# Kernel optimization log

Hardware: AMD Instinct MI355X
Metric: run time of the kernel (lower is better)

The kernel has to match this reference:

```python
import jax, jax.numpy as jnp
import numpy as np

SR = 44100
DUR = 2.0
DS = 64
IN_GAIN = 10.0 ** (5.2 / 20.0)


def design_lr4_ir(freq, sr, n_taps=512):
    wc = np.tan(np.pi * freq / sr)
    wc2 = wc * wc
    root2 = np.sqrt(2.0)
    denom = 1 + root2 * wc + wc2
    b_lp = np.array([wc2 / denom, 2 * wc2 / denom, wc2 / denom])
    a_lp = np.array([1.0, 2 * (wc2 - 1) / denom, (1 - root2 * wc + wc2) / denom])
    b_hp = np.array([1 / denom, -2 / denom, 1 / denom])
    a_hp = np.array([1.0, 2 * (wc2 - 1) / denom, (1 - root2 * wc + wc2) / denom])
    b_lp4 = np.convolve(b_lp, b_lp); a_lp4 = np.convolve(a_lp, a_lp)
    b_hp4 = np.convolve(b_hp, b_hp); a_hp4 = np.convolve(a_hp, a_hp)
    def lfilter(b, a, x):
        y = np.zeros_like(x)
        for n in range(len(x)):
            acc = 0.0
            for i in range(len(b)):
                if n - i >= 0:
                    acc += b[i] * x[n - i]
            for i in range(1, len(a)):
                if n - i >= 0:
                    acc -= a[i] * y[n - i]
            y[n] = acc
        return y
    imp = np.zeros(n_taps); imp[0] = 1.0
    return lfilter(b_lp4, a_lp4, imp), lfilter(b_hp4, a_hp4, imp)


def _fir(x, w):
    # x: [B,C,T], w: flipped IR [K]; causal (left) padding, same filter per channel (grouped)
    K = w.shape[0]; C = x.shape[1]
    xp = jnp.pad(x, ((0, 0), (0, 0), (K - 1, 0)))
    kern = jnp.broadcast_to(w.reshape(1, 1, K), (C, 1, K))
    return jax.lax.conv_general_dilated(xp, kern, (1,), 'VALID',
                                        dimension_numbers=('NCH', 'OIH', 'NCH'),
                                        feature_group_count=C)


def _conv1d(x, w, b, pad, dil):
    y = jax.lax.conv_general_dilated(x, w, (1,), [(pad, pad)], rhs_dilation=(dil,),
                                     dimension_numbers=('NCH', 'OIH', 'NCH'))
    return y + b[None, :, None]


def _knee(x, thr, slope, k):
    diff = x - thr
    g_knee = slope * (diff + k / 2) ** 2 / (2 * k)
    return jnp.where(jnp.abs(diff) <= k / 2, g_knee,
                     jnp.where(diff > k / 2, slope * diff, jnp.zeros_like(x)))


def _forward(audio, params, rel_alphas, knee_db, ir_low_lp, ir_low_hp, ir_high_lp, ir_high_hp,
             w0, b0, w1, b1, w2, b2, w3, b3, w4, b4):
    batch, C, T = audio.shape
    audio_in = audio * IN_GAIN
    ott = params[:, -7:]
    amount = ott[:, 0][:, None, None]
    # 3-band LR4 crossover via 512-tap FIRs
    low = _fir(audio_in, ir_low_lp)
    m_h = _fir(audio_in, ir_low_hp)
    mid = _fir(m_h, ir_high_lp)
    high = _fir(m_h, ir_high_hp)
    bands = jnp.stack([high, mid, low], axis=1)            # [B,3,2,T]
    b_flat = bands.reshape(batch * 3, C, T)
    x_sq = jnp.mean(b_flat ** 2, axis=1, keepdims=True)    # [B3,1,T]
    Tc = T // DS
    x_rms = jnp.sqrt(x_sq[..., :Tc * DS].reshape(batch * 3, 1, Tc, DS).mean(-1) + 1e-7)
    # release-only envelope follower via cummax trick (faithful to torch code incl. repeat order)
    rel = jnp.repeat(rel_alphas, batch).reshape(-1, 1, 1)
    k = 1.0 - rel
    idx = jnp.arange(Tc, dtype=x_rms.dtype)
    kp = k ** idx
    ki = k ** (-idx)
    env_c = jax.lax.cummax(x_rms * ki, axis=2) * kp        # [B3,1,Tc]
    # linear interp back to T (align_corners=True)
    pos = jnp.arange(T, dtype=jnp.float32) * ((Tc - 1) / (T - 1))
    i0 = jnp.clip(jnp.floor(pos).astype(jnp.int32), 0, Tc - 2)
    frac = pos - i0.astype(jnp.float32)
    env = jnp.take(env_c, i0, axis=2) * (1 - frac) + jnp.take(env_c, i0 + 1, axis=2) * frac
    env_db = 20.0 * jnp.log10(env + 1e-7).reshape(batch, 3, T)
    t_a = jnp.stack([ott[:, 3], ott[:, 2], ott[:, 1]], axis=1)[..., None]
    t_b = jnp.stack([ott[:, 6], ott[:, 5], ott[:, 4]], axis=1)[..., None]
    above_slopes = jnp.array([1.0, 1.0 - 1 / 66.7, 1.0 - 1 / 66.7], jnp.float32).reshape(1, 3, 1)
    below_slope = jnp.float32(1.0 - 1.0 / 4.17)
    g_db = -_knee(env_db, t_a, above_slopes, knee_db) + _knee(-env_db, -t_b, below_slope, knee_db)
    out_gains = jnp.array([10.3, 5.7, 10.3], jnp.float32).reshape(1, 3, 1)
    total_g = 10.0 ** (jnp.clip(g_db + out_gains, -80.0, 40.0) / 20.0)
    combined = (bands * total_g[:, :, None, :]).sum(axis=1)  # [B,2,T]
    g = lambda z: jax.nn.gelu(z, approximate=False)
    r = g(_conv1d(combined, w0, b0, 1, 1))
    r = g(_conv1d(r, w1, b1, 2, 2))
    r = g(_conv1d(r, w2, b2, 4, 4))
    r = g(_conv1d(r, w3, b3, 8, 8))
    res = _conv1d(r, w4, b4, 1, 1)
    return (1.0 - amount) * audio + amount * (combined + res)


def setup_inputs() -> dict:
    B = 8
    T = int(SR * DUR)
    key = jax.random.key(0)
    ks = jax.random.split(key, 16)
    audio = jax.random.normal(ks[0], (B, 2, T), jnp.float32)
    amount = jax.random.uniform(ks[1], (B, 1), jnp.float32)
    thr = jax.random.uniform(ks[2], (B, 6), jnp.float32, minval=-40.0, maxval=0.0)
    params = jnp.concatenate([amount, thr], axis=1)
    ir_lp1, ir_hp1 = design_lr4_ir(88.3, SR)
    ir_lp2, ir_hp2 = design_lr4_ir(2500.0, SR)
    flip = lambda ir: jnp.asarray(ir[::-1].copy(), jnp.float32)
    sr_c = SR / DS
    rel_alphas = jnp.asarray(1.0 - np.exp(-1.0 / (sr_c * np.array([132.0, 282.0, 282.0]) / 1000.0)), jnp.float32)
    knee_db = jnp.float32(3.0)
    shapes = [(64, 2, 3), (64, 64, 3), (64, 64, 3), (64, 64, 3), (2, 64, 3)]
    out = {
        'audio': audio, 'params': params, 'rel_alphas': rel_alphas, 'knee_db': knee_db,
        'ir_low_lp': flip(ir_lp1), 'ir_low_hp': flip(ir_hp1),
        'ir_high_lp': flip(ir_lp2), 'ir_high_hp': flip(ir_hp2),
    }
    for i, (o, ci, kk) in enumerate(shapes):
        bound = 1.0 / np.sqrt(ci * kk)
        scale = 0.01 if i == len(shapes) - 1 else 1.0
        out[f'w{i}'] = jax.random.uniform(ks[4 + 2 * i], (o, ci, kk), jnp.float32, -bound, bound) * scale
        out[f'b{i}'] = jax.random.uniform(ks[5 + 2 * i], (o,), jnp.float32, -bound, bound) * scale
    return out


def reference(audio, params, rel_alphas, knee_db, ir_low_lp, ir_low_hp, ir_high_lp, ir_high_hp,
              w0, b0, w1, b1, w2, b2, w3, b3, w4, b4):
    return _forward(audio, params, rel_alphas, knee_db, ir_low_lp, ir_low_hp, ir_high_lp, ir_high_hp,
                    w0, b0, w1, b1, w2, b2, w3, b3, w4, b4)
```

## Files before the change

kernel.cpp:

```cpp
#include <hip/hip_runtime.h>
#include <math.h>

#define NT 88200
#define NB 8
#define TC 1378

static constexpr float IN_GAIN_F = 1.8197008586099834f;

#define OFF_A0    3072
#define OFF_A4    4096
#define OFF_ABF   5632
#define OFF_BANDS 24064
#define OFF_XRMS  4257664
#define OFF_ENV   4290736
#define OFF_WHL   4290736

typedef __attribute__((ext_vector_type(8))) short short8v;
typedef __attribute__((ext_vector_type(4))) short short4v;
typedef __attribute__((ext_vector_type(2))) unsigned int uint2v;
typedef __attribute__((ext_vector_type(4))) float float4v;
typedef __attribute__((ext_vector_type(16))) float float16v;
typedef __attribute__((ext_vector_type(8))) _Float16 half8v;

__device__ __forceinline__ float gelu_h(float x) {
  float s = __builtin_amdgcn_fmed3f(fmaf(0.28366667f, x, 0.5f), 0.f, 1.f);
  return x * s;
}
__device__ __forceinline__ short f2bf(float x) {
  unsigned int u = __float_as_uint(x);
  u += 0x7fffu + ((u >> 16) & 1u);
  return (short)(u >> 16);
}
__device__ __forceinline__ short f2fh(float x) {
  union { _Float16 h; short s; } u;
  u.h = (_Float16)x;
  return u.s;
}
__device__ __forceinline__ half8v s2h(short8v s) {
  union { short8v s; half8v h; } u;
  u.s = s;
  return u.h;
}
__device__ __forceinline__ unsigned int cvt_pk_bf16(float lo, float hi) {
  unsigned int d;
  asm("v_cvt_pk_bf16_f32 %0, %1, %2" : "=v"(d) : "v"(lo), "v"(hi));
  return d;
}

__global__ __launch_bounds__(256) void k_prep(
    const float* __restrict__ irLL, const float* __restrict__ irLH,
    const float* __restrict__ irHL, const float* __restrict__ irHH,
    const float* __restrict__ w0, const float* __restrict__ w1,
    const float* __restrict__ w2, const float* __restrict__ w3,
    const float* __restrict__ w4, float* __restrict__ ws)
{
  int gid = blockIdx.x * 256 + threadIdx.x;
  int task = blockIdx.y;
  if (task == 0) {
    short* whl = (short*)(ws + OFF_WHL);
    if (gid < 3072) {
      int band = gid >> 10, j = gid & 1023;
      float v = 0.f;
      if (j < 1023) {
        if (band == 2) {
          v = (j >= 511) ? irLL[j - 511] : 0.f;
        } else {
          const float* wb = (band == 0) ? irHH : irHL;
          int lo = j - 511; if (lo < 0) lo = 0;
          int hi = (j < 511) ? j : 511;
          float acc = 0.f;
          for (int i = lo; i <= hi; ++i) acc += irLH[i] * wb[j - i];
          v = acc;
        }
      }
      whl[band * 1152 + 64 + j] = f2fh(v);
    } else if (gid < 4608) {
      int z = gid - 3072;
      int entry;
      if (z < 384) {
        int band = z >> 7, r = z & 127;
        entry = band * 1152 + (r < 64 ? r : 1024 + r);
      } else {
        entry = 3 * 1152 + (z - 384);
      }
      whl[entry] = 0;
    }
  } else if (task == 1) {
    if (gid >= 2048) return;
    int wq = gid >> 9;
    int lane = (gid >> 3) & 63;
    int j = gid & 7;
    int l16 = lane & 15, q = lane >> 4;
    int m = wq * 16 + l16;
    int K = q * 8 + j;
    float val = (K < 6) ? w0[(m * 2 + (K & 1)) * 3 + (K >> 1)] : 0.f;
    ((short*)(ws + OFF_A0))[gid] = f2bf(val);
  } else if (task == 2) {
    if (gid >= 3072) return;
    int s = gid >> 9;
    int lane = (gid - s * 512) >> 3;
    int j = gid & 7;
    int m = lane & 15, q = lane >> 4;
    int K = s * 32 + q * 8 + j;
    int k = K >> 6, ic = K & 63;
    float val = (m < 2) ? w4[(m * 64 + ic) * 3 + k] : 0.f;
    ((short*)(ws + OFF_A4))[gid] = f2bf(val);
  } else if (task == 6) {
    for (int r = 0; r < 3; ++r) {
      int i = gid * 3 + r;
      if (i < 24 * TC) ws[OFF_XRMS + i] = 0.f;
    }
  } else {
    int l = task - 3;
    if (gid >= 12288) return;
    const float* wl = (l == 0) ? w1 : (l == 1) ? w2 : w3;
    int ocg = gid / 6144;
    int rem = gid - ocg * 6144;
    int s = rem / 512;
    int rem2 = rem - s * 512;
    int lane = rem2 >> 3;
    int j = gid & 7;
    int m = ocg * 32 + (lane & 31);
    int k = s * 16 + ((lane >> 5) << 3) + j;
    int tap = k >> 6, ic = k & 63;
    short* ap = (short*)(ws + OFF_ABF);
    ap[l * 12288 + gid] = f2bf(wl[(m * 64 + ic) * 3 + tap]);
  }
}

#define FT 320
__global__ __launch_bounds__(256) void k_firm(const float* __restrict__ audio,
                                              float* __restrict__ ws)
{
  __shared__ short xh[4][1360];
  __shared__ __align__(16) short wt[4608];
  __shared__ float ssum[3][5];
  int bc = blockIdx.x, tile = blockIdx.y;
  int t0b = tile * FT;
  int tid = threadIdx.x;
  if (tid < 15) ssum[tid / 5][tid % 5] = 0.f;
  const uint4* wsrc = (const uint4*)((const short*)(ws + OFF_WHL));
  uint4* wdst = (uint4*)wt;
  for (int i = tid; i < 576; i += 256) wdst[i] = wsrc[i];
  const float* x = audio + bc * NT;
  for (int i = tid; i < 1363; i += 256) {
    int g = t0b - 1022 + i;
    float v = (g >= 0 && g < NT) ? x[g] * IN_GAIN_F : 0.f;
    short h = f2fh(v);
#pragma unroll
    for (int c = 0; c < 4; ++c) {
      int idx = i - c;
      if (idx >= 0 && idx < 1360) xh[c][idx] = h;
    }
  }
  __syncthreads();

  int wave = tid >> 6, lane = tid & 63;
  int q = lane >> 4, l16 = lane & 15;
  int band = (l16 >= 10) ? 2 : (l16 >= 5 ? 1 : 0);
  if (l16 == 15) band = 3;
  int u = l16 - band * 5;
  const short* pAh = wt + band * 1152 + 64 + q * 8 - u * 16;
  int c = l16 & 3;
  int xoff = wave * 80 + q * 8 + ((l16 >> 2) << 2);
  const short* pBh = &xh[c][xoff];
  float4v a0 = {0.f, 0.f, 0.f, 0.f};
#pragma unroll 2
  for (int s = 0; s < 34; ++s) {
    half8v ah = *(const half8v*)(pAh + 32 * s);
    short4v bh0 = *(const short4v*)(pBh + 32 * s);
    short4v bh1 = *(const short4v*)(pBh + 32 * s + 4);
    short8v bh = __builtin_shufflevector(bh0, bh1, 0, 1, 2, 3, 4, 5, 6, 7);
    a0 = __builtin_amdgcn_mfma_f32_16x16x32_f16(ah, s2h(bh), a0, 0, 0, 0);
  }
  float acc[4];
#pragma unroll
  for (int r = 0; r < 4; ++r) acc[r] = a0[r];

  int b = bc >> 1, ch = bc & 1;
  float* bands = ws + OFF_BANDS;
#pragma unroll
  for (int r = 0; r < 4; ++r) {
    int m = q * 4 + r;
    if (m < 15) {
      int bnd = (m >= 10) ? 2 : (m >= 5 ? 1 : 0);
      int uu = m - bnd * 5;
      int t = t0b + wave * 80 + uu * 16 + l16;
      if (t < NT) bands[((b * 3 + bnd) * 2 + ch) * NT + t] = acc[r];
    }
  }

  float s2[4];
#pragma unroll
  for (int r = 0; r < 4; ++r) {
    int m = q * 4 + r;
    s2[r] = (m < 15) ? acc[r] * acc[r] : 0.f;
  }
#pragma unroll
  for (int mask = 1; mask < 16; mask <<= 1)
#pragma unroll
    for (int r = 0; r < 4; ++r)
      s2[r] += __shfl_xor(s2[r], mask, 16);
  if (l16 == 0) {
#pragma unroll
    for (int r = 0; r < 4; ++r) {
      int m = q * 4 + r;
      if (m < 15) {
        int bnd = (m >= 10) ? 2 : (m >= 5 ? 1 : 0);
        int uu = m - bnd * 5;
        int jloc = (wave * 80 + uu * 16) >> 6;
        atomicAdd(&ssum[bnd][jloc], s2[r]);
      }
    }
  }
  __syncthreads();
  if (tid < 15) {
    int bnd = tid / 5, jl = tid - bnd * 5;
    int jg = tile * 5 + jl;
    if (jg < TC) atomicAdd(&ws[OFF_XRMS + (b * 3 + bnd) * TC + jg], ssum[bnd][jl]);
  }
}

__global__ __launch_bounds__(256) void k_scan(const float* __restrict__ rel_alphas,
                                              float* __restrict__ ws)
{
  __shared__ float pA[256], pB[256];
  int row = blockIdx.x;
  int tid = threadIdx.x;
  float kdec = 1.f - rel_alphas[row >> 3];
  const float* xr = ws + OFF_XRMS + row * TC;
  float v[6];
  int base = tid * 6;
#pragma unroll
  for (int s = 0; s < 6; ++s) {
    int j = base + s;
    v[s] = (j < TC) ? sqrtf(xr[j] * (0.5f / 64.f) + 1e-7f) : 0.f;
  }
  float r = v[0];
#pragma unroll
  for (int s = 1; s < 6; ++s) r = fmaxf(v[s], r * kdec);
  pA[tid] = r;
  __syncthreads();
  float k2 = kdec * kdec, k3 = k2 * kdec;
  float kp = k3 * k3;
  float* in = pA; float* outp = pB;
  for (int off = 1; off < 256; off <<= 1) {
    float val = in[tid];
    if (tid >= off) val = fmaxf(val, in[tid - off] * kp);
    outp[tid] = val;
    kp *= kp;
    __syncthreads();
    float* tmp = in; in = outp; outp = tmp;
  }
  float* env = ws + OFF_ENV + row * TC;
  float rr;
  if (tid > 0) {
    float carry = in[tid - 1];
    rr = fmaxf(v[0], carry * kdec);
  } else {
    rr = v[0];
  }
  if (base < TC) env[base] = rr;
#pragma unroll
  for (int s = 1; s < 6; ++s) {
    rr = fmaxf(v[s], rr * kdec);
    if (base + s < TC) env[base + s] = rr;
  }
}

#define PITCH 72
#define SPAN 256
#define TILE 224

__device__ __forceinline__ void mfma_layer32(const short* in, short* outb,
    const short* __restrict__ apk, const float* __restrict__ bias,
    const int d, int t0, int ocg, int posg, int lane)
{
  int l32 = lane & 31, hi = lane >> 5;
  float16v acc;
#pragma unroll
  for (int g = 0; g < 4; ++g) {
    float4 bv = *(const float4*)&bias[ocg * 32 + hi * 4 + g * 8];
    acc[4 * g + 0] = bv.x; acc[4 * g + 1] = bv.y;
    acc[4 * g + 2] = bv.z; acc[4 * g + 3] = bv.w;
  }
  int rbase = posg * 32 + l32;
  int rlo = rbase - d; rlo = rlo < 0 ? 0 : rlo;
  int rhi = rbase + d; rhi = rhi > SPAN - 1 ? SPAN - 1 : rhi;
  const short* pLo  = in + rlo * PITCH + hi * 8;
  const short* pMid = in + rbase * PITCH + hi * 8;
  const short* pHi  = in + rhi * PITCH + hi * 8;
  const short* ap = apk + (ocg * 12 * 64 + lane) * 8;
#pragma unroll
  for (int s = 0; s < 12; ++s) {
    short8v a = *(const short8v*)(ap + s * 512);
    int tap = s >> 2;
    const short* p = (tap == 0) ? pLo : (tap == 1) ? pMid : pHi;
    short8v bf = *(const short8v*)(p + (s & 3) * 16);
    acc = __builtin_amdgcn_mfma_f32_32x32x16_bf16(a, bf, acc, 0, 0, 0);
  }
  int t = t0 - 16 + rbase;
  bool z = (t < 0) | (t >= NT);
  short* wp = outb + rbase * PITCH + ocg * 32 + hi * 4;
#pragma unroll
  for (int g = 0; g < 4; ++g) {
    uint2v r;
    r[0] = cvt_pk_bf16(gelu_h(acc[4 * g + 0]), gelu_h(acc[4 * g + 1]));
    r[1] = cvt_pk_bf16(gelu_h(acc[4 * g + 2]), gelu_h(acc[4 * g + 3]));
    r[0] = z ? 0u : r[0];
    r[1] = z ? 0u : r[1];
    *(uint2v*)(wp + g * 8) = r;
  }
}

__global__ __launch_bounds__(1024, 8) void k_convnet(
    const float* __restrict__ audio, const float* __restrict__ params,
    const float* __restrict__ kneep,
    const float* __restrict__ b0, const float* __restrict__ b1,
    const float* __restrict__ b2, const float* __restrict__ b3,
    const float* __restrict__ b4, const float* __restrict__ ws,
    float* __restrict__ out)
{
  __shared__ float cmb[2][SPAN];
  __shared__ __align__(16) char ubuf[SPAN * 8 * 2];
  __shared__ __align__(16) short actA[SPAN * PITCH];
  __shared__ __align__(16) short actB[SPAN * PITCH];
  short (*bfL0)[8] = (short(*)[8])ubuf;
  int tile = blockIdx.x, b = blockIdx.y;
  int t0 = tile * TILE;
  int tid = threadIdx.x;
  int wave = tid >> 6, lane = tid & 63;

  if (tid < SPAN) {
    int t = t0 - 16 + tid;
    float c0 = 0.f, c1 = 0.f;
    if (t >= 0 && t < NT) {
      const float* env = ws + OFF_ENV;
      const float* bands = ws + OFF_BANDS;
      float knee = kneep[0];
      float halfk = 0.5f * knee;
      float inv2k = 1.f / (2.f * knee);
      const float scale = (float)(1377.0 / 88199.0);
      float pos_f = (float)t * scale;
      int i0 = (int)floorf(pos_f);
      i0 = i0 < 0 ? 0 : (i0 > TC - 2 ? TC - 2 : i0);
      float frac = pos_f - (float)i0;
      const int tacol[3] = {3, 2, 1};
      const int tbcol[3] = {6, 5, 4};
      const float asl[3] = {1.f, (float)(1.0 - 1.0 / 66.7), (float)(1.0 - 1.0 / 66.7)};
      const float bsl = (float)(1.0 - 1.0 / 4.17);
      const float og[3] = {10.3f, 5.7f, 10.3f};
#pragma unroll
      for (int band = 0; band < 3; ++band) {
        int row = b * 3 + band;
        float e = env[row * TC + i0] * (1.f - frac) + env[row * TC + i0 + 1] * frac;
        float edb = 6.0205999132796239f * __builtin_amdgcn_logf(e + 1e-7f);
        float ta = params[b * 7 + tacol[band]];
        float tb = params[b * 7 + tbcol[band]];
        float d1 = edb - ta;
        float gk1 = asl[band] * (d1 + halfk) * (d1 + halfk) * inv2k;
        float ka = (fabsf(d1) <= halfk) ? gk1 : (d1 > halfk ? asl[band] * d1 : 0.f);
        float d2 = tb - edb;
        float gk2 = bsl * (d2 + halfk) * (d2 + halfk) * inv2k;
        float kb = (fabsf(d2) <= halfk) ? gk2 : (d2 > halfk ? bsl * d2 : 0.f);
        float gdb = -ka + kb + og[band];
        gdb = fminf(fmaxf(gdb, -80.f), 40.f);
        float g = __builtin_amdgcn_exp2f(gdb * 0.16609640474436812f);
        c0 += bands[(row * 2 + 0) * NT + t] * g;
        c1 += bands[(row * 2 + 1) * NT + t] * g;
      }
    }
    cmb[0][tid] = c0;
    cmb[1][tid] = c1;
  }
  __syncthreads();

  for (int i = tid; i < SPAN * 8; i += 1024) {
    int r = i >> 3, j = i & 7;
    short v = 0;
    if (j < 6) {
      int k = j >> 1, ic = j & 1;
      int src = r - 1 + k;
      if (src >= 0 && src < SPAN) v = f2bf(cmb[ic][src]);
    }
    bfL0[r][j] = v;
  }
  __syncthreads();

  int quad = lane >> 4, l16 = lane & 15;

  {
    int wq = wave & 3, half = wave >> 2;
    const short* ap0 = (const short*)(ws + OFF_A0);
    short8v a0 = *(const short8v*)&ap0[(wq * 64 + lane) * 8];
    float4 bv = *(const float4*)&b0[wq * 16 + quad * 4];
    float4v acc[4];
#pragma unroll
    for (int n = 0; n < 4; ++n) { acc[n][0] = bv.x; acc[n][1] = bv.y; acc[n][2] = bv.z; acc[n][3] = bv.w; }
    short8v zf = {0, 0, 0, 0, 0, 0, 0, 0};
#pragma unroll
    for (int n = 0; n < 4; ++n) {
      int row = (half * 4 + n) * 16 + l16;
      short8v bf = (quad == 0) ? *(const short8v*)&bfL0[row][0] : zf;
      acc[n] = __builtin_amdgcn_mfma_f32_16x16x32_bf16(a0, bf, acc[n], 0, 0, 0);
    }
    int ocb = wq * 16 + quad * 4;
#pragma unroll
    for (int n = 0; n < 4; ++n) {
      int p = (half * 4 + n) * 16 + l16;
      int t = t0 - 16 + p;
      bool z = (t < 0) | (t >= NT);
      uint2v r;
      r[0] = cvt_pk_bf16(gelu_h(acc[n][0]), gelu_h(acc[n][1]));
      r[1] = cvt_pk_bf16(gelu_h(acc[n][2]), gelu_h(acc[n][3]));
      r[0] = z ? 0u : r[0];
      r[1] = z ? 0u : r[1];
      *(uint2v*)&actA[p * PITCH + ocb] = r;
    }
  }
  __syncthreads();

  int ocg = wave & 1, posg = wave >> 1;
  const short* apk = (const short*)(ws + OFF_ABF);
  mfma_layer32(actA, actB, apk,          b1, 2, t0, ocg, posg, lane);
  __syncthreads();
  mfma_layer32(actB, actA, apk + 12288,  b2, 4, t0, ocg, posg, lane);
  __syncthreads();
  mfma_layer32(actA, actB, apk + 24576,  b3, 8, t0, ocg, posg, lane);
  __syncthreads();

  if (wave < 14) {
    const short* ap4 = (const short*)(ws + OFF_A4);
    float4v acc = {0.f, 0.f, 0.f, 0.f};
    if (quad == 0) { acc[0] = b4[0]; acc[1] = b4[1]; }
#pragma unroll
    for (int s = 0; s < 6; ++s) {
      short8v a4 = *(const short8v*)&ap4[(s * 64 + lane) * 8];
      int kt = s >> 1;
      int ic0 = (s & 1) * 32 + quad * 8;
      int row = 16 + wave * 16 + l16 + kt - 1;
      short8v bf = *(const short8v*)&actB[row * PITCH + ic0];
      acc = __builtin_amdgcn_mfma_f32_16x16x32_bf16(a4, bf, acc, 0, 0, 0);
    }
    if (quad == 0) {
      int t = t0 + wave * 16 + l16;
      if (t < NT) {
        float amt = params[b * 7];
#pragma unroll
        for (int r = 0; r < 2; ++r) {
          float aud = audio[(b * 2 + r) * NT + t];
          out[(b * 2 + r) * NT + t] =
              (1.f - amt) * aud + amt * (cmb[r][16 + wave * 16 + l16] + acc[r]);
        }
      }
    }
  }
}

extern "C" void kernel_launch(void* const* d_in, const int* in_sizes, int n_in,
                              void* d_out, int out_size, void* d_ws, size_t ws_size,
                              hipStream_t stream)
{
  (void)in_sizes; (void)n_in; (void)out_size; (void)ws_size;
  const float* audio = (const float*)d_in[0];
  const float* params = (const float*)d_in[1];
  const float* rel   = (const float*)d_in[2];
  const float* knee  = (const float*)d_in[3];
  const float* irLL  = (const float*)d_in[4];
  const float* irLH  = (const float*)d_in[5];
  const float* irHL  = (const float*)d_in[6];
  const float* irHH  = (const float*)d_in[7];
  const float* w0 = (const float*)d_in[8];  const float* b0 = (const float*)d_in[9];
  const float* w1 = (const float*)d_in[10]; const float* b1 = (const float*)d_in[11];
  const float* w2 = (const float*)d_in[12]; const float* b2 = (const float*)d_in[13];
  const float* w3 = (const float*)d_in[14]; const float* b3 = (const float*)d_in[15];
  const float* w4 = (const float*)d_in[16]; const float* b4 = (const float*)d_in[17];
  float* out = (float*)d_out;
  float* ws  = (float*)d_ws;

  hipLaunchKernelGGL(k_prep, dim3(48, 7), dim3(256), 0, stream,
                     irLL, irLH, irHL, irHH, w0, w1, w2, w3, w4, ws);
  hipLaunchKernelGGL(k_firm, dim3(16, 276), dim3(256), 0, stream, audio, ws);
  hipLaunchKernelGGL(k_scan, dim3(24), dim3(256), 0, stream, rel, ws);
  hipLaunchKernelGGL(k_convnet, dim3(394, 8), dim3(1024), 0, stream,
                     audio, params, knee, b0, b1, b2, b3, b4, ws, out);
}
```

Measured before the change: 276.1 us.

## Split MFMA accumulator chains, batch weight loads, parallelize band combine per channel

```diff
diff --git a/kernel.cpp b/kernel.cpp
--- a/kernel.cpp
+++ b/kernel.cpp
@@ -165,17 +165,23 @@
   int xoff = wave * 80 + q * 8 + ((l16 >> 2) << 2);
   const short* pBh = &xh[c][xoff];
   float4v a0 = {0.f, 0.f, 0.f, 0.f};
+  float4v a1 = {0.f, 0.f, 0.f, 0.f};
 #pragma unroll 2
-  for (int s = 0; s < 34; ++s) {
-    half8v ah = *(const half8v*)(pAh + 32 * s);
-    short4v bh0 = *(const short4v*)(pBh + 32 * s);
-    short4v bh1 = *(const short4v*)(pBh + 32 * s + 4);
-    short8v bh = __builtin_shufflevector(bh0, bh1, 0, 1, 2, 3, 4, 5, 6, 7);
-    a0 = __builtin_amdgcn_mfma_f32_16x16x32_f16(ah, s2h(bh), a0, 0, 0, 0);
+  for (int s = 0; s < 34; s += 2) {
+    half8v ah0 = *(const half8v*)(pAh + 32 * s);
+    half8v ah1 = *(const half8v*)(pAh + 32 * (s + 1));
+    short4v b00 = *(const short4v*)(pBh + 32 * s);
+    short4v b01 = *(const short4v*)(pBh + 32 * s + 4);
+    short4v b10 = *(const short4v*)(pBh + 32 * (s + 1));
+    short4v b11 = *(const short4v*)(pBh + 32 * (s + 1) + 4);
+    short8v bh0 = __builtin_shufflevector(b00, b01, 0, 1, 2, 3, 4, 5, 6, 7);
+    short8v bh1 = __builtin_shufflevector(b10, b11, 0, 1, 2, 3, 4, 5, 6, 7);
+    a0 = __builtin_amdgcn_mfma_f32_16x16x32_f16(ah0, s2h(bh0), a0, 0, 0, 0);
+    a1 = __builtin_amdgcn_mfma_f32_16x16x32_f16(ah1, s2h(bh1), a1, 0, 0, 0);
   }
   float acc[4];
 #pragma unroll
-  for (int r = 0; r < 4; ++r) acc[r] = a0[r];
+  for (int r = 0; r < 4; ++r) acc[r] = a0[r] + a1[r];
 
   int b = bc >> 1, ch = bc & 1;
   float* bands = ws + OFF_BANDS;
@@ -291,14 +297,25 @@
   const short* pMid = in + rbase * PITCH + hi * 8;
   const short* pHi  = in + rhi * PITCH + hi * 8;
   const short* ap = apk + (ocg * 12 * 64 + lane) * 8;
-#pragma unroll
-  for (int s = 0; s < 12; ++s) {
-    short8v a = *(const short8v*)(ap + s * 512);
-    int tap = s >> 2;
-    const short* p = (tap == 0) ? pLo : (tap == 1) ? pMid : pHi;
+
+  short8v af[6];
+#pragma unroll
+  for (int k = 0; k < 6; ++k) af[k] = *(const short8v*)(ap + k * 512);
+#pragma unroll
+  for (int s = 0; s < 6; ++s) {
+    const short* p = (s < 4) ? pLo : pMid;
     short8v bf = *(const short8v*)(p + (s & 3) * 16);
-    acc = __builtin_amdgcn_mfma_f32_32x32x16_bf16(a, bf, acc, 0, 0, 0);
-  }
+    acc = __builtin_amdgcn_mfma_f32_32x32x16_bf16(af[s], bf, acc, 0, 0, 0);
+  }
+#pragma unroll
+  for (int k = 0; k < 6; ++k) af[k] = *(const short8v*)(ap + (k + 6) * 512);
+#pragma unroll
+  for (int s = 6; s < 12; ++s) {
+    const short* p = (s < 8) ? pMid : pHi;
+    short8v bf = *(const short8v*)(p + (s & 3) * 16);
+    acc = __builtin_amdgcn_mfma_f32_32x32x16_bf16(af[s - 6], bf, acc, 0, 0, 0);
+  }
+
   int t = t0 - 16 + rbase;
   bool z = (t < 0) | (t >= NT);
   short* wp = outb + rbase * PITCH + ocg * 32 + hi * 4;
@@ -331,9 +348,11 @@
   int tid = threadIdx.x;
   int wave = tid >> 6, lane = tid & 63;
 
-  if (tid < SPAN) {
-    int t = t0 - 16 + tid;
-    float c0 = 0.f, c1 = 0.f;
+  if (tid < 2 * SPAN) {
+    int ch = tid >> 8;
+    int pos = tid & (SPAN - 1);
+    int t = t0 - 16 + pos;
+    float cc = 0.f;
     if (t >= 0 && t < NT) {
       const float* env = ws + OFF_ENV;
       const float* bands = ws + OFF_BANDS;
@@ -366,12 +385,10 @@
         float gdb = -ka + kb + og[band];
         gdb = fminf(fmaxf(gdb, -80.f), 40.f);
         float g = __builtin_amdgcn_exp2f(gdb * 0.16609640474436812f);
-        c0 += bands[(row * 2 + 0) * NT + t] * g;
-        c1 += bands[(row * 2 + 1) * NT + t] * g;
+        cc += bands[(row * 2 + ch) * NT + t] * g;
       }
     }
-    cmb[0][tid] = c0;
-    cmb[1][tid] = c1;
+    cmb[ch][pos] = cc;
   }
   __syncthreads();
 
@@ -431,16 +448,18 @@
 
   if (wave < 14) {
     const short* ap4 = (const short*)(ws + OFF_A4);
+    short8v a4f[6];
+#pragma unroll
+    for (int s = 0; s < 6; ++s) a4f[s] = *(const short8v*)&ap4[(s * 64 + lane) * 8];
     float4v acc = {0.f, 0.f, 0.f, 0.f};
     if (quad == 0) { acc[0] = b4[0]; acc[1] = b4[1]; }
 #pragma unroll
     for (int s = 0; s < 6; ++s) {
-      short8v a4 = *(const short8v*)&ap4[(s * 64 + lane) * 8];
       int kt = s >> 1;
       int ic0 = (s & 1) * 32 + quad * 8;
       int row = 16 + wave * 16 + l16 + kt - 1;
       short8v bf = *(const short8v*)&actB[row * PITCH + ic0];
-      acc = __builtin_amdgcn_mfma_f32_16x16x32_bf16(a4, bf, acc, 0, 0, 0);
+      acc = __builtin_amdgcn_mfma_f32_16x16x32_bf16(a4f[s], bf, acc, 0, 0, 0);
     }
     if (quad == 0) {
       int t = t0 + wave * 16 + l16;
```

Measured after the change: 271.4 us. About the same (-1.7%).
